# Optimization experiments

Hardware: AMD Instinct MI355X
Metric: run time of the kernel (lower is better)

The kernel has to match this reference:

```python
import jax, jax.numpy as jnp
import numpy as np

EPS = 1e-6
MAX_ITER = 3

def skew(w):
    z = jnp.zeros_like(w[:, 0])
    return jnp.stack([
        jnp.stack([z, -w[:, 2], w[:, 1]], -1),
        jnp.stack([w[:, 2], z, -w[:, 0]], -1),
        jnp.stack([-w[:, 1], w[:, 0], z], -1)], -2)

def twist2mat(w):
    # Rodrigues formula, w: [B,3] -> R: [B,3,3]
    theta = jnp.linalg.norm(w, axis=-1, keepdims=True) + 1e-12
    axis = w / theta
    Km = skew(axis)
    th = theta[..., None]
    I = jnp.eye(3, dtype=w.dtype)
    return I + jnp.sin(th) * Km + (1.0 - jnp.cos(th)) * (Km @ Km)

def sobel_gradient(img, normalize=True):
    # replicate-pad + 3x3 Sobel, img: [B,C,H,W]
    p = jnp.pad(img, ((0, 0), (0, 0), (1, 1), (1, 1)), mode='edge')
    tl = p[..., :-2, :-2]; tc = p[..., :-2, 1:-1]; tr = p[..., :-2, 2:]
    ml = p[..., 1:-1, :-2]; mr = p[..., 1:-1, 2:]
    bl = p[..., 2:, :-2]; bc = p[..., 2:, 1:-1]; br = p[..., 2:, 2:]
    dx = (tr - tl) + 2.0 * (mr - ml) + (br - bl)
    dy = (bl - tl) + 2.0 * (bc - tc) + (br - tr)
    if normalize:
        mag = jnp.sqrt(dx * dx + dy * dy + 1e-8)
        dx, dy = dx / mag, dy / mag
    return dx, dy

def _bilinear_one(F, u, v):
    # F: [C,H,W]; u,v: [H,W] pixel coords; border padding (grid_sample-like)
    C, H, W = F.shape
    u = jnp.clip(u, 0.0, W - 1.0)
    v = jnp.clip(v, 0.0, H - 1.0)
    x0 = jnp.floor(u); y0 = jnp.floor(v)
    wx = u - x0; wy = v - y0
    x0i = x0.astype(jnp.int32); y0i = y0.astype(jnp.int32)
    x1i = jnp.minimum(x0i + 1, W - 1); y1i = jnp.minimum(y0i + 1, H - 1)
    g = lambda yi, xi: F[:, yi, xi]  # advanced-index gather -> [C,H,W]
    return (g(y0i, x0i) * (1 - wx) * (1 - wy) + g(y0i, x1i) * wx * (1 - wy)
            + g(y1i, x0i) * (1 - wx) * wy + g(y1i, x1i) * wx * wy)

def warp_features(F, u, v):
    # F: [B,C,H,W]; u,v: [B,1,H,W]
    return jax.vmap(_bilinear_one)(F, u[:, 0], v[:, 0])

def generate_xy_grid(B, H, W, K):
    fx, fy, cx, cy = [K[:, i].reshape(B, 1, 1, 1) for i in range(4)]
    uu, vv = jnp.meshgrid(jnp.arange(W, dtype=K.dtype), jnp.arange(H, dtype=K.dtype))
    px = (uu[None, None] - cx) / fx
    py = (vv[None, None] - cy) / fy
    return px, py  # [B,1,H,W] each

def batch_warp_inverse_depth(px, py, invD0, R, t, K):
    B, _, H, W = px.shape
    xy1 = jnp.concatenate([px, py, jnp.ones_like(px)], 1).reshape(B, 3, -1)
    warped = R @ xy1 + t[:, :, None] * invD0.reshape(B, 1, -1)
    x_, y_, s_ = warped[:, 0], warped[:, 1], warped[:, 2]
    fx, fy, cx, cy = [K[:, i].reshape(B, 1) for i in range(4)]
    u_ = (x_ / s_ * fx + cx).reshape(B, 1, H, W)
    v_ = (y_ / s_ * fy + cy).reshape(B, 1, H, W)
    inv_z = invD0 / s_.reshape(B, 1, H, W)
    return u_, v_, inv_z

def check_occ(inv_z_buffer, invD1, u, v, thres=0.1):
    B, _, H, W = invD1.shape
    inv_z_warped = warp_features(invD1, u, v)
    inlier = inv_z_buffer > inv_z_warped - thres
    inview = (u > 0) & (u < W) & (v > 0) & (v < H)
    return ~(inlier & inview)  # [B,1,H,W] bool

def compute_jacobian_warping(invD, K, px, py):
    # linearized at origin (pose=None branch)
    B, _, H, W = invD.shape
    x = px.reshape(B, -1); y = py.reshape(B, -1); d = invD.reshape(B, -1)
    O = jnp.zeros_like(x)
    xy = x * y
    dx_dp = jnp.stack([-xy, 1.0 + x * x, -y, d, O, -d * x], -1)
    dy_dp = jnp.stack([-(1.0 + y * y), xy, x, O, d, -d * y], -1)
    fx = K[:, 0].reshape(B, 1, 1); fy = K[:, 1].reshape(B, 1, 1)
    return dx_dp * fx, dy_dp * fy  # [B,HW,6] each

def lev_mar_H(JtWJ):
    diag = jnp.eye(6, dtype=JtWJ.dtype)
    trace = jnp.trace(JtWJ, axis1=1, axis2=2)
    return JtWJ + (trace * 1e-6)[:, None, None] * diag

def forward(twist0, x0, x1, invD0, invD1, sigma0, sigma1, K):
    B, C, H, W = x0.shape
    N = H * W
    dtype = x0.dtype
    R = twist2mat(twist0[:, :3])
    t = twist0[:, 3:]
    px, py = generate_xy_grid(B, H, W, K)
    # inverse-compositional: template Jacobian precomputed once
    Jf_x, Jf_y = sobel_gradient(x0, normalize=True)
    Jx_p, Jy_p = compute_jacobian_warping(invD0, K, px, py)
    J = (Jf_x.reshape(B, C, N, 1) * Jx_p.reshape(B, 1, N, 6)
         + Jf_y.reshape(B, C, N, 1) * Jy_p.reshape(B, 1, N, 6))  # [B,C,N,6]
    for _ in range(MAX_ITER):
        u_w, v_w, inv_z = batch_warp_inverse_depth(px, py, invD0, R, t, K)
        occ = check_occ(inv_z, invD1, u_w, v_w)
        f_r = warp_features(x1, u_w, v_w)
        sigma_r = warp_features(sigma1, u_w, v_w)
        res = f_r - x0
        sigma = jnp.sqrt(sigma_r * sigma_r + sigma0 * sigma0)
        wres = jnp.where(occ, EPS, res / sigma)  # [B,C,H,W]
        valid = (~occ).reshape(B, 1, N, 1).astype(dtype)
        Jw = (J / sigma.reshape(B, C, N, 1) * valid).reshape(B, C * N, 6)
        r = jnp.where(occ, 0.0, wres).reshape(B, C * N)
        JtWJ = jnp.einsum('bnk,bnl->bkl', Jw, Jw)
        Rhs = jnp.einsum('bnk,bn->bk', Jw, r)[..., None]
        xi = jnp.linalg.solve(lev_mar_H(JtWJ), Rhs)  # [B,6,1]
        d_R = twist2mat(-xi[:, :3, 0])
        d_t = -(d_R @ xi[:, 3:])
        t = (R @ d_t)[:, :, 0] + t
        R = R @ d_R
    return jnp.concatenate([R.reshape(B, 9), t], axis=1)  # [B,12]

def setup_inputs() -> dict:
    key = jax.random.key(0)
    ks = jax.random.split(key, 7)
    B, C, H, W = 8, 16, 240, 320
    twist0 = jax.random.normal(ks[0], (B, 6), jnp.float32) * 0.01
    x0 = jax.random.normal(ks[1], (B, C, H, W), jnp.float32)
    x1 = jax.random.normal(ks[2], (B, C, H, W), jnp.float32)
    invD0 = jax.random.uniform(ks[3], (B, 1, H, W), jnp.float32, 0.1, 1.0)
    invD1 = jax.random.uniform(ks[4], (B, 1, H, W), jnp.float32, 0.1, 1.0)
    sigma0 = jax.random.uniform(ks[5], (B, C, H, W), jnp.float32, 0.1, 1.0)
    sigma1 = jax.random.uniform(ks[6], (B, C, H, W), jnp.float32, 0.1, 1.0)
    Kmat = jnp.tile(jnp.array([[0.8 * W, 0.8 * W, W / 2.0, H / 2.0]], jnp.float32), (B, 1))
    return dict(twist0=twist0, x0=x0, x1=x1, invD0=invD0, invD1=invD1,
                sigma0=sigma0, sigma1=sigma1, K=Kmat)

def reference(twist0, x0, x1, invD0, invD1, sigma0, sigma1, K):
    return forward(twist0, x0, x1, invD0, invD1, sigma0, sigma1, K)
```

## Files before the change

kernel.cpp:

```cpp
#include <hip/hip_runtime.h>
#include <hip/hip_fp16.h>

#define B_ 8
#define C_ 16
#define H_ 240
#define W_ 320
#define N_ (H_*W_)

__device__ __forceinline__ void twist2mat_dev(float w0, float w1, float w2, float R[9]) {
    float th = sqrtf(w0*w0 + w1*w1 + w2*w2) + 1e-12f;
    float ax = w0/th, ay = w1/th, az = w2/th;
    float s = sinf(th), c = cosf(th), ic = 1.0f - c;
    R[0] = 1.0f + ic*(ax*ax - 1.0f);
    R[1] = -s*az + ic*ax*ay;
    R[2] =  s*ay + ic*ax*az;
    R[3] =  s*az + ic*ax*ay;
    R[4] = 1.0f + ic*(ay*ay - 1.0f);
    R[5] = -s*ax + ic*ay*az;
    R[6] = -s*ay + ic*ax*az;
    R[7] =  s*ax + ic*ay*az;
    R[8] = 1.0f + ic*(az*az - 1.0f);
}

__device__ __forceinline__ unsigned pack_h2(float a, float b) {
    __half2 h = __floats2half2_rn(a, b);
    return *reinterpret_cast<unsigned*>(&h);
}
__device__ __forceinline__ float2 unpack_h2(unsigned u) {
    __half2 h = *reinterpret_cast<__half2*>(&u);
    return __half22float2(h);
}

__device__ __forceinline__ void solve_update(const float* __restrict__ ac, float R[9], float t[3]) {
    float M[6][7];
    {
        int idx = 0;
        #pragma unroll
        for (int k = 0; k < 6; k++)
            #pragma unroll
            for (int l = k; l < 6; l++) { M[k][l] = ac[idx]; M[l][k] = ac[idx]; idx++; }
    }
    const float trace = M[0][0]+M[1][1]+M[2][2]+M[3][3]+M[4][4]+M[5][5];
    const float lam = trace * 1e-6f;
    #pragma unroll
    for (int i = 0; i < 6; i++) { M[i][i] += lam; M[i][6] = ac[21+i]; }

    #pragma unroll
    for (int k = 0; k < 6; k++) {
        const float inv = 1.0f / M[k][k];
        #pragma unroll
        for (int i = k+1; i < 6; i++) {
            const float f = M[i][k] * inv;
            #pragma unroll
            for (int j = k; j < 7; j++) M[i][j] -= f * M[k][j];
        }
    }
    float xi[6];
    #pragma unroll
    for (int i = 5; i >= 0; i--) {
        float s = M[i][6];
        #pragma unroll
        for (int j = i+1; j < 6; j++) s -= M[i][j]*xi[j];
        xi[i] = s / M[i][i];
    }

    float dR[9];
    twist2mat_dev(-xi[0], -xi[1], -xi[2], dR);
    const float dt0 = -(dR[0]*xi[3] + dR[1]*xi[4] + dR[2]*xi[5]);
    const float dt1 = -(dR[3]*xi[3] + dR[4]*xi[4] + dR[5]*xi[5]);
    const float dt2 = -(dR[6]*xi[3] + dR[7]*xi[4] + dR[8]*xi[5]);

    const float nt0 = R[0]*dt0 + R[1]*dt1 + R[2]*dt2 + t[0];
    const float nt1 = R[3]*dt0 + R[4]*dt1 + R[5]*dt2 + t[1];
    const float nt2 = R[6]*dt0 + R[7]*dt1 + R[8]*dt2 + t[2];
    float nR[9];
    #pragma unroll
    for (int i = 0; i < 3; i++)
        #pragma unroll
        for (int j = 0; j < 3; j++)
            nR[i*3+j] = R[i*3+0]*dR[0*3+j] + R[i*3+1]*dR[1*3+j] + R[i*3+2]*dR[2*3+j];
    #pragma unroll
    for (int i = 0; i < 9; i++) R[i] = nR[i];
    t[0] = nt0; t[1] = nt1; t[2] = nt2;
}

__device__ __forceinline__ void build_RT(const float* __restrict__ twist0,
                                         const float* __restrict__ accum,
                                         int b, int iters, float R[9], float t[3]) {
    const float* w = twist0 + b*6;
    twist2mat_dev(w[0], w[1], w[2], R);
    t[0] = w[3]; t[1] = w[4]; t[2] = w[5];
    for (int j = 0; j < iters; j++)
        solve_update(accum + (size_t)(j*B_ + b)*27, R, t);
}

__launch_bounds__(256)
__global__ void precompute_kernel(const float* __restrict__ x0, const float* __restrict__ x1,
                                  const float* __restrict__ sigma0, const float* __restrict__ sigma1,
                                  uint4* __restrict__ P0h, uint4* __restrict__ X1S1h,
                                  float* __restrict__ accum)
{
    if (blockIdx.x == 0 && blockIdx.y == 0 && blockIdx.z == 0) {
        for (int k = threadIdx.x; k < 3*B_*27; k += 256) accum[k] = 0.0f;
    }
    const int b  = blockIdx.z;
    const int cg = blockIdx.y;
    const int base_pix = blockIdx.x * 256;
    const int pix = base_pix + threadIdx.x;
    const int h0 = base_pix / W_;

    __shared__ float lds[4][4][W_];

    const size_t cbase = ((size_t)(b*C_) + cg*4) * N_;

    float s0a[4], x1a[4], s1a[4];
    #pragma unroll
    for (int i = 0; i < 4; i++) {
        const size_t o = cbase + (size_t)i*N_ + pix;
        s0a[i] = sigma0[o];
        x1a[i] = x1[o];
        s1a[i] = sigma1[o];
    }

    #pragma unroll
    for (int k = 0; k < 5; k++) {
        const int idx = threadIdx.x + k*256;
        const int ch  = idx / 320;
        const int rem = idx - ch*320;
        const int row = rem / 80;
        const int c4  = rem - row*80;
        const int src_r = min(max(h0 - 1 + row, 0), H_ - 1);
        const float4 v = *reinterpret_cast<const float4*>(
            x0 + cbase + (size_t)ch*N_ + (size_t)src_r*W_ + c4*4);
        *reinterpret_cast<float4*>(&lds[ch][row][c4*4]) = v;
    }
    __syncthreads();

    const int h = pix / W_;
    const int w = pix - h*W_;
    const int lr = h - (h0 - 1);
    const int wm = max(w-1, 0), wp = min(w+1, W_-1);

    unsigned gq[4], xq[4], qq[4];
    #pragma unroll
    for (int i = 0; i < 4; i++) {
        const float* rT = lds[i][lr-1];
        const float* rM = lds[i][lr];
        const float* rB = lds[i][lr+1];
        const float tl = rT[wm], tc_ = rT[w], tr = rT[wp];
        const float ml = rM[wm], ctr = rM[w], mr = rM[wp];
        const float bl = rB[wm], bc_ = rB[w], br = rB[wp];
        const float dx = tr - tl + 2.0f*(mr - ml) + (br - bl);
        const float dy = bl - tl + 2.0f*(bc_ - tc_) + (br - tr);
        const float mag = sqrtf(dx*dx + dy*dy + 1e-8f);
        gq[i] = pack_h2(dx/mag, dy/mag);
        xq[i] = pack_h2(ctr, s0a[i]*s0a[i]);
        qq[i] = pack_h2(x1a[i], s1a[i]);
    }

    uint4 A;  A.x = gq[0];  A.y = xq[0];  A.z = gq[1];  A.w = xq[1];
    uint4 Bw; Bw.x = gq[2]; Bw.y = xq[2]; Bw.z = gq[3]; Bw.w = xq[3];
    uint4 Q;  Q.x = qq[0];  Q.y = qq[1];  Q.z = qq[2];  Q.w = qq[3];
    P0h[((size_t)(b*8 + cg*2  ))*N_ + pix] = A;
    P0h[((size_t)(b*8 + cg*2+1))*N_ + pix] = Bw;
    X1S1h[((size_t)(b*4 + cg))*N_ + pix] = Q;
}

__device__ __forceinline__ void accum_pixel(int pix,
                                            const float Rm[9], const float tv[3],
                                            float fx, float fy, float cx, float cy,
                                            const uint4* __restrict__ P0b,
                                            const uint4* __restrict__ X1S1b,
                                            const float* __restrict__ d0,
                                            const float* __restrict__ dz,
                                            float* __restrict__ acc)
{
    const int h = pix / W_;
    const int w = pix - h*W_;

    const float px = ((float)w - cx) / fx;
    const float py = ((float)h - cy) / fy;
    const float d  = d0[pix];

    const float x_ = Rm[0]*px + Rm[1]*py + Rm[2] + tv[0]*d;
    const float y_ = Rm[3]*px + Rm[4]*py + Rm[5] + tv[1]*d;
    const float s_ = Rm[6]*px + Rm[7]*py + Rm[8] + tv[2]*d;
    const float u = x_/s_*fx + cx;
    const float v = y_/s_*fy + cy;
    const float inv_z = d / s_;

    const float uc = fminf(fmaxf(u, 0.0f), (float)(W_-1));
    const float vc = fminf(fmaxf(v, 0.0f), (float)(H_-1));
    const float x0f = floorf(uc), y0f = floorf(vc);
    const float wx = uc - x0f, wy = vc - y0f;
    const int x0i = (int)x0f, y0i = (int)y0f;
    const int x1i = min(x0i+1, W_-1), y1i = min(y0i+1, H_-1);
    const float w00 = (1.0f-wx)*(1.0f-wy), w01 = wx*(1.0f-wy);
    const float w10 = (1.0f-wx)*wy,        w11 = wx*wy;
    const int i00 = y0i*W_+x0i, i01 = y0i*W_+x1i, i10 = y1i*W_+x0i, i11 = y1i*W_+x1i;

    const float zw = dz[i00]*w00 + dz[i01]*w01 + dz[i10]*w10 + dz[i11]*w11;
    const bool inlier = inv_z > zw - 0.1f;
    const bool inview = (u > 0.0f) && (u < (float)W_) && (v > 0.0f) && (v < (float)H_);
    const bool valid  = inlier && inview;

    if (!valid) return;

    const float xy = px*py;
    const float Av[6] = { -xy*fx, (1.0f+px*px)*fx, -py*fx, d*fx, 0.0f, -d*px*fx };
    const float Bv[6] = { -(1.0f+py*py)*fy, xy*fy, px*fy, 0.0f, d*fy, -d*py*fy };

    float Swxx=0.f, Swxy=0.f, Swyy=0.f, Srx=0.f, Sry=0.f;

#define CH(gword, xword, t00, t01, t10, t11) { \
    const float2 g  = unpack_h2(gword); \
    const float2 xs = unpack_h2(xword); \
    const float2 a00 = unpack_h2(t00), a01 = unpack_h2(t01), \
                 a10 = unpack_h2(t10), a11 = unpack_h2(t11); \
    const float fr = a00.x*w00 + a01.x*w01 + a10.x*w10 + a11.x*w11; \
    const float sr = a00.y*w00 + a01.y*w01 + a10.y*w10 + a11.y*w11; \
    const float inv_s2 = 1.0f/(sr*sr + xs.y); \
    const float res = fr - xs.x; \
    const float gxw = g.x*inv_s2, gyw = g.y*inv_s2; \
    Swxx += g.x*gxw; Swxy += g.x*gyw; Swyy += g.y*gyw; \
    Srx  += res*gxw; Sry  += res*gyw; }

    #pragma unroll
    for (int cg = 0; cg < 4; cg++) {
        const uint4 pA = P0b[(size_t)(cg*2  )*N_ + pix];
        const uint4 pB = P0b[(size_t)(cg*2+1)*N_ + pix];
        const uint4* xsb = X1S1b + (size_t)cg*N_;
        const uint4 q00 = xsb[i00], q01 = xsb[i01], q10 = xsb[i10], q11 = xsb[i11];
        CH(pA.x, pA.y, q00.x, q01.x, q10.x, q11.x)
        CH(pA.z, pA.w, q00.y, q01.y, q10.y, q11.y)
        CH(pB.x, pB.y, q00.z, q01.z, q10.z, q11.z)
        CH(pB.z, pB.w, q00.w, q01.w, q10.w, q11.w)
    }
#undef CH

    int idx = 0;
    #pragma unroll
    for (int k = 0; k < 6; k++) {
        #pragma unroll
        for (int l = k; l < 6; l++) {
            acc[idx++] += Swxx*Av[k]*Av[l] + Swxy*(Av[k]*Bv[l] + Bv[k]*Av[l]) + Swyy*Bv[k]*Bv[l];
        }
    }
    #pragma unroll
    for (int k = 0; k < 6; k++) acc[21+k] += Srx*Av[k] + Sry*Bv[k];
}

__launch_bounds__(256)
__global__ void iter_kernel(const uint4* __restrict__ P0h, const uint4* __restrict__ X1S1h,
                            const float* __restrict__ invD0, const float* __restrict__ invD1,
                            const float* __restrict__ Kmat, const float* __restrict__ twist0,
                            float* __restrict__ accum, int it)
{
    const int b = blockIdx.y;
    const int pix0 = blockIdx.x * 512 + threadIdx.x;

    float Rm[9], tv[3];
    build_RT(twist0, accum, b, it, Rm, tv);

    const float fx = Kmat[b*4+0], fy = Kmat[b*4+1], cx = Kmat[b*4+2], cy = Kmat[b*4+3];

    float acc[27];
    #pragma unroll
    for (int j = 0; j < 27; j++) acc[j] = 0.0f;

    const uint4* P0b   = P0h   + (size_t)b*8*N_;
    const uint4* X1S1b = X1S1h + (size_t)b*4*N_;
    const float* d0 = invD0 + b*N_;
    const float* dz = invD1 + b*N_;

    accum_pixel(pix0,       Rm, tv, fx, fy, cx, cy, P0b, X1S1b, d0, dz, acc);
    accum_pixel(pix0 + 256, Rm, tv, fx, fy, cx, cy, P0b, X1S1b, d0, dz, acc);

    const int lane = threadIdx.x & 63;
    const int wave = threadIdx.x >> 6;
    __shared__ float red[4][27];
    #pragma unroll
    for (int j = 0; j < 27; j++) {
        float vv = acc[j];
        vv += __shfl_down(vv, 32);
        vv += __shfl_down(vv, 16);
        vv += __shfl_down(vv, 8);
        vv += __shfl_down(vv, 4);
        vv += __shfl_down(vv, 2);
        vv += __shfl_down(vv, 1);
        if (lane == 0) red[wave][j] = vv;
    }
    __syncthreads();
    if (threadIdx.x < 27) {
        float s = red[0][threadIdx.x] + red[1][threadIdx.x] + red[2][threadIdx.x] + red[3][threadIdx.x];
        atomicAdd(&accum[(size_t)(it*B_ + b)*27 + threadIdx.x], s);
    }
}

__global__ void finalize_kernel(const float* __restrict__ twist0, const float* __restrict__ accum,
                                float* __restrict__ out)
{
    const int b = threadIdx.x;
    if (b >= B_) return;
    float Rm[9], tv[3];
    build_RT(twist0, accum, b, 3, Rm, tv);
    float* ob = out + b*12;
    #pragma unroll
    for (int i = 0; i < 9; i++) ob[i] = Rm[i];
    ob[9] = tv[0]; ob[10] = tv[1]; ob[11] = tv[2];
}

extern "C" void kernel_launch(void* const* d_in, const int* in_sizes, int n_in,
                              void* d_out, int out_size, void* d_ws, size_t ws_size,
                              hipStream_t stream) {
    const float* twist0 = (const float*)d_in[0];
    const float* x0     = (const float*)d_in[1];
    const float* x1     = (const float*)d_in[2];
    const float* invD0  = (const float*)d_in[3];
    const float* invD1  = (const float*)d_in[4];
    const float* sigma0 = (const float*)d_in[5];
    const float* sigma1 = (const float*)d_in[6];
    const float* Kmat   = (const float*)d_in[7];
    float* out = (float*)d_out;

    const size_t p0_bytes = (size_t)B_*8*N_*sizeof(uint4);
    const size_t xs_bytes = (size_t)B_*4*N_*sizeof(uint4);

    uint4* P0h   = (uint4*)d_ws;
    uint4* X1S1h = (uint4*)((char*)d_ws + p0_bytes);
    float* accum = (float*)((char*)d_ws + p0_bytes + xs_bytes);

    hipLaunchKernelGGL(precompute_kernel, dim3(N_/256, 4, B_), dim3(256), 0, stream,
                       x0, x1, sigma0, sigma1, P0h, X1S1h, accum);

    dim3 grid(N_/512, B_);
    for (int it = 0; it < 3; ++it) {
        hipLaunchKernelGGL(iter_kernel, grid, dim3(256), 0, stream,
                           P0h, X1S1h, invD0, invD1, Kmat, twist0, accum, it);
    }
    hipLaunchKernelGGL(finalize_kernel, dim3(1), dim3(64), 0, stream, twist0, accum, out);
}
```

Baseline: 335.6 us.

## Split iteration kernel across channel groups with four pixels per thread

The iteration kernel now gives each block one channel group (4 of 16 channels) instead of all channels, and each thread handles four pixels instead of two. Grid rows become batch times channel groups, while the pixel blocks per row are halved. Each thread holds fewer live gather loads per pixel, which may help occupancy and latency hiding. The cost is that the geometry, projection and Jacobian work is repeated four times per pixel, and the 6x6 accumulation plus atomic reduction now runs per channel group.

```diff
diff --git a/kernel.cpp b/kernel.cpp
--- a/kernel.cpp
+++ b/kernel.cpp
@@ -166,14 +166,14 @@
     X1S1h[((size_t)(b*4 + cg))*N_ + pix] = Q;
 }
 
-__device__ __forceinline__ void accum_pixel(int pix,
-                                            const float Rm[9], const float tv[3],
-                                            float fx, float fy, float cx, float cy,
-                                            const uint4* __restrict__ P0b,
-                                            const uint4* __restrict__ X1S1b,
-                                            const float* __restrict__ d0,
-                                            const float* __restrict__ dz,
-                                            float* __restrict__ acc)
+__device__ __forceinline__ void accum_pixel_cg(int pix,
+                                               const float Rm[9], const float tv[3],
+                                               float fx, float fy, float cx, float cy,
+                                               const uint4* __restrict__ P0cg,
+                                               const uint4* __restrict__ X1cg,
+                                               const float* __restrict__ d0,
+                                               const float* __restrict__ dz,
+                                               float* __restrict__ acc)
 {
     const int h = pix / W_;
     const int w = pix - h*W_;
@@ -225,12 +225,10 @@
     Swxx += g.x*gxw; Swxy += g.x*gyw; Swyy += g.y*gyw; \
     Srx  += res*gxw; Sry  += res*gyw; }
 
-    #pragma unroll
-    for (int cg = 0; cg < 4; cg++) {
-        const uint4 pA = P0b[(size_t)(cg*2  )*N_ + pix];
-        const uint4 pB = P0b[(size_t)(cg*2+1)*N_ + pix];
-        const uint4* xsb = X1S1b + (size_t)cg*N_;
-        const uint4 q00 = xsb[i00], q01 = xsb[i01], q10 = xsb[i10], q11 = xsb[i11];
+    {
+        const uint4 pA = P0cg[pix];
+        const uint4 pB = P0cg[N_ + pix];
+        const uint4 q00 = X1cg[i00], q01 = X1cg[i01], q10 = X1cg[i10], q11 = X1cg[i11];
         CH(pA.x, pA.y, q00.x, q01.x, q10.x, q11.x)
         CH(pA.z, pA.w, q00.y, q01.y, q10.y, q11.y)
         CH(pB.x, pB.y, q00.z, q01.z, q10.z, q11.z)
@@ -256,8 +254,9 @@
                             const float* __restrict__ Kmat, const float* __restrict__ twist0,
                             float* __restrict__ accum, int it)
 {
-    const int b = blockIdx.y;
-    const int pix0 = blockIdx.x * 512 + threadIdx.x;
+    const int b  = blockIdx.y >> 2;
+    const int cg = blockIdx.y & 3;
+    const int pix0 = blockIdx.x * 1024 + threadIdx.x;
 
     float Rm[9], tv[3];
     build_RT(twist0, accum, b, it, Rm, tv);
@@ -268,13 +267,15 @@
     #pragma unroll
     for (int j = 0; j < 27; j++) acc[j] = 0.0f;
 
-    const uint4* P0b   = P0h   + (size_t)b*8*N_;
-    const uint4* X1S1b = X1S1h + (size_t)b*4*N_;
+    const uint4* P0cg = P0h   + (size_t)(b*8 + cg*2)*N_;
+    const uint4* X1cg = X1S1h + (size_t)(b*4 + cg  )*N_;
     const float* d0 = invD0 + b*N_;
     const float* dz = invD1 + b*N_;
 
-    accum_pixel(pix0,       Rm, tv, fx, fy, cx, cy, P0b, X1S1b, d0, dz, acc);
-    accum_pixel(pix0 + 256, Rm, tv, fx, fy, cx, cy, P0b, X1S1b, d0, dz, acc);
+    accum_pixel_cg(pix0,       Rm, tv, fx, fy, cx, cy, P0cg, X1cg, d0, dz, acc);
+    accum_pixel_cg(pix0 + 256, Rm, tv, fx, fy, cx, cy, P0cg, X1cg, d0, dz, acc);
+    accum_pixel_cg(pix0 + 512, Rm, tv, fx, fy, cx, cy, P0cg, X1cg, d0, dz, acc);
+    accum_pixel_cg(pix0 + 768, Rm, tv, fx, fy, cx, cy, P0cg, X1cg, d0, dz, acc);
 
     const int lane = threadIdx.x & 63;
     const int wave = threadIdx.x >> 6;
@@ -333,7 +334,7 @@
     hipLaunchKernelGGL(precompute_kernel, dim3(N_/256, 4, B_), dim3(256), 0, stream,
                        x0, x1, sigma0, sigma1, P0h, X1S1h, accum);
 
-    dim3 grid(N_/512, B_);
+    dim3 grid(N_/1024, B_*4);
     for (int it = 0; it < 3; ++it) {
         hipLaunchKernelGGL(iter_kernel, grid, dim3(256), 0, stream,
                            P0h, X1S1h, invD0, invD1, Kmat, twist0, accum, it);
```

Result: slower. 381.7 us (+13.7%).

## Interleave two pixels per thread and replace validity branch with mask

Applied to the files above, without the earlier changes.

The per-pixel function that handled two pixels one after another, with an early return for invalid pixels, is split into warp setup and per-channel accumulation. Both pixels' gathers are now issued together, which raises memory-level parallelism. The validity branch becomes a multiplicative mask, so invalid pixels still do all loads and math but divergence is removed. This raises register pressure and adds redundant gathers for invalid pixels.

```diff
diff --git a/kernel.cpp b/kernel.cpp
--- a/kernel.cpp
+++ b/kernel.cpp
@@ -166,88 +166,54 @@
     X1S1h[((size_t)(b*4 + cg))*N_ + pix] = Q;
 }
 
-__device__ __forceinline__ void accum_pixel(int pix,
-                                            const float Rm[9], const float tv[3],
-                                            float fx, float fy, float cx, float cy,
-                                            const uint4* __restrict__ P0b,
-                                            const uint4* __restrict__ X1S1b,
-                                            const float* __restrict__ d0,
-                                            const float* __restrict__ dz,
-                                            float* __restrict__ acc)
-{
+struct Warp {
+    int i00, i01, i10, i11;
+    float w00, w01, w10, w11;
+    float inv_z;
+    float px, py;
+    bool  inview;
+};
+
+__device__ __forceinline__ Warp make_warp(int pix, float d, const float Rm[9], const float tv[3],
+                                          float fx, float fy, float cx, float cy) {
+    Warp W;
     const int h = pix / W_;
     const int w = pix - h*W_;
-
-    const float px = ((float)w - cx) / fx;
-    const float py = ((float)h - cy) / fy;
-    const float d  = d0[pix];
-
-    const float x_ = Rm[0]*px + Rm[1]*py + Rm[2] + tv[0]*d;
-    const float y_ = Rm[3]*px + Rm[4]*py + Rm[5] + tv[1]*d;
-    const float s_ = Rm[6]*px + Rm[7]*py + Rm[8] + tv[2]*d;
+    W.px = ((float)w - cx) / fx;
+    W.py = ((float)h - cy) / fy;
+    const float x_ = Rm[0]*W.px + Rm[1]*W.py + Rm[2] + tv[0]*d;
+    const float y_ = Rm[3]*W.px + Rm[4]*W.py + Rm[5] + tv[1]*d;
+    const float s_ = Rm[6]*W.px + Rm[7]*W.py + Rm[8] + tv[2]*d;
     const float u = x_/s_*fx + cx;
     const float v = y_/s_*fy + cy;
-    const float inv_z = d / s_;
-
+    W.inv_z = d / s_;
     const float uc = fminf(fmaxf(u, 0.0f), (float)(W_-1));
     const float vc = fminf(fmaxf(v, 0.0f), (float)(H_-1));
     const float x0f = floorf(uc), y0f = floorf(vc);
     const float wx = uc - x0f, wy = vc - y0f;
     const int x0i = (int)x0f, y0i = (int)y0f;
     const int x1i = min(x0i+1, W_-1), y1i = min(y0i+1, H_-1);
-    const float w00 = (1.0f-wx)*(1.0f-wy), w01 = wx*(1.0f-wy);
-    const float w10 = (1.0f-wx)*wy,        w11 = wx*wy;
-    const int i00 = y0i*W_+x0i, i01 = y0i*W_+x1i, i10 = y1i*W_+x0i, i11 = y1i*W_+x1i;
-
-    const float zw = dz[i00]*w00 + dz[i01]*w01 + dz[i10]*w10 + dz[i11]*w11;
-    const bool inlier = inv_z > zw - 0.1f;
-    const bool inview = (u > 0.0f) && (u < (float)W_) && (v > 0.0f) && (v < (float)H_);
-    const bool valid  = inlier && inview;
-
-    if (!valid) return;
-
-    const float xy = px*py;
-    const float Av[6] = { -xy*fx, (1.0f+px*px)*fx, -py*fx, d*fx, 0.0f, -d*px*fx };
-    const float Bv[6] = { -(1.0f+py*py)*fy, xy*fy, px*fy, 0.0f, d*fy, -d*py*fy };
-
-    float Swxx=0.f, Swxy=0.f, Swyy=0.f, Srx=0.f, Sry=0.f;
-
-#define CH(gword, xword, t00, t01, t10, t11) { \
-    const float2 g  = unpack_h2(gword); \
-    const float2 xs = unpack_h2(xword); \
-    const float2 a00 = unpack_h2(t00), a01 = unpack_h2(t01), \
-                 a10 = unpack_h2(t10), a11 = unpack_h2(t11); \
-    const float fr = a00.x*w00 + a01.x*w01 + a10.x*w10 + a11.x*w11; \
-    const float sr = a00.y*w00 + a01.y*w01 + a10.y*w10 + a11.y*w11; \
-    const float inv_s2 = 1.0f/(sr*sr + xs.y); \
-    const float res = fr - xs.x; \
-    const float gxw = g.x*inv_s2, gyw = g.y*inv_s2; \
-    Swxx += g.x*gxw; Swxy += g.x*gyw; Swyy += g.y*gyw; \
-    Srx  += res*gxw; Sry  += res*gyw; }
-
-    #pragma unroll
-    for (int cg = 0; cg < 4; cg++) {
-        const uint4 pA = P0b[(size_t)(cg*2  )*N_ + pix];
-        const uint4 pB = P0b[(size_t)(cg*2+1)*N_ + pix];
-        const uint4* xsb = X1S1b + (size_t)cg*N_;
-        const uint4 q00 = xsb[i00], q01 = xsb[i01], q10 = xsb[i10], q11 = xsb[i11];
-        CH(pA.x, pA.y, q00.x, q01.x, q10.x, q11.x)
-        CH(pA.z, pA.w, q00.y, q01.y, q10.y, q11.y)
-        CH(pB.x, pB.y, q00.z, q01.z, q10.z, q11.z)
-        CH(pB.z, pB.w, q00.w, q01.w, q10.w, q11.w)
-    }
-#undef CH
-
-    int idx = 0;
-    #pragma unroll
-    for (int k = 0; k < 6; k++) {
-        #pragma unroll
-        for (int l = k; l < 6; l++) {
-            acc[idx++] += Swxx*Av[k]*Av[l] + Swxy*(Av[k]*Bv[l] + Bv[k]*Av[l]) + Swyy*Bv[k]*Bv[l];
-        }
-    }
-    #pragma unroll
-    for (int k = 0; k < 6; k++) acc[21+k] += Srx*Av[k] + Sry*Bv[k];
+    W.w00 = (1.0f-wx)*(1.0f-wy); W.w01 = wx*(1.0f-wy);
+    W.w10 = (1.0f-wx)*wy;        W.w11 = wx*wy;
+    W.i00 = y0i*W_+x0i; W.i01 = y0i*W_+x1i; W.i10 = y1i*W_+x0i; W.i11 = y1i*W_+x1i;
+    W.inview = (u > 0.0f) && (u < (float)W_) && (v > 0.0f) && (v < (float)H_);
+    return W;
+}
+
+__device__ __forceinline__ void ch_accum(const Warp& W, float S[5],
+                                         unsigned gword, unsigned xword,
+                                         unsigned t00, unsigned t01, unsigned t10, unsigned t11) {
+    const float2 g  = unpack_h2(gword);
+    const float2 xs = unpack_h2(xword);
+    const float2 a00 = unpack_h2(t00), a01 = unpack_h2(t01),
+                 a10 = unpack_h2(t10), a11 = unpack_h2(t11);
+    const float fr = a00.x*W.w00 + a01.x*W.w01 + a10.x*W.w10 + a11.x*W.w11;
+    const float sr = a00.y*W.w00 + a01.y*W.w01 + a10.y*W.w10 + a11.y*W.w11;
+    const float inv_s2 = 1.0f/(sr*sr + xs.y);
+    const float res = fr - xs.x;
+    const float gxw = g.x*inv_s2, gyw = g.y*inv_s2;
+    S[0] += g.x*gxw; S[1] += g.x*gyw; S[2] += g.y*gyw;
+    S[3] += res*gxw; S[4] += res*gyw;
 }
 
 __launch_bounds__(256)
@@ -257,24 +223,89 @@
                             float* __restrict__ accum, int it)
 {
     const int b = blockIdx.y;
-    const int pix0 = blockIdx.x * 512 + threadIdx.x;
+    const int pixA = blockIdx.x * 512 + threadIdx.x;
+    const int pixB = pixA + 256;
 
     float Rm[9], tv[3];
     build_RT(twist0, accum, b, it, Rm, tv);
 
     const float fx = Kmat[b*4+0], fy = Kmat[b*4+1], cx = Kmat[b*4+2], cy = Kmat[b*4+3];
 
-    float acc[27];
-    #pragma unroll
-    for (int j = 0; j < 27; j++) acc[j] = 0.0f;
-
+    const float* d0 = invD0 + b*N_;
+    const float* dz = invD1 + b*N_;
     const uint4* P0b   = P0h   + (size_t)b*8*N_;
     const uint4* X1S1b = X1S1h + (size_t)b*4*N_;
-    const float* d0 = invD0 + b*N_;
-    const float* dz = invD1 + b*N_;
-
-    accum_pixel(pix0,       Rm, tv, fx, fy, cx, cy, P0b, X1S1b, d0, dz, acc);
-    accum_pixel(pix0 + 256, Rm, tv, fx, fy, cx, cy, P0b, X1S1b, d0, dz, acc);
+
+    const float dA = d0[pixA];
+    const float dB = d0[pixB];
+
+    const Warp A = make_warp(pixA, dA, Rm, tv, fx, fy, cx, cy);
+    const Warp B = make_warp(pixB, dB, Rm, tv, fx, fy, cx, cy);
+
+    const float zA00 = dz[A.i00], zA01 = dz[A.i01], zA10 = dz[A.i10], zA11 = dz[A.i11];
+    const float zB00 = dz[B.i00], zB01 = dz[B.i01], zB10 = dz[B.i10], zB11 = dz[B.i11];
+    const float zwA = zA00*A.w00 + zA01*A.w01 + zA10*A.w10 + zA11*A.w11;
+    const float zwB = zB00*B.w00 + zB01*B.w01 + zB10*B.w10 + zB11*B.w11;
+    const float vmA = (A.inv_z > zwA - 0.1f && A.inview) ? 1.0f : 0.0f;
+    const float vmB = (B.inv_z > zwB - 0.1f && B.inview) ? 1.0f : 0.0f;
+
+    float SA[5] = {0.f,0.f,0.f,0.f,0.f};
+    float SB[5] = {0.f,0.f,0.f,0.f,0.f};
+
+    #pragma unroll
+    for (int cg = 0; cg < 4; cg++) {
+        const uint4 pAa = P0b[(size_t)(cg*2  )*N_ + pixA];
+        const uint4 pAb = P0b[(size_t)(cg*2+1)*N_ + pixA];
+        const uint4 pBa = P0b[(size_t)(cg*2  )*N_ + pixB];
+        const uint4 pBb = P0b[(size_t)(cg*2+1)*N_ + pixB];
+        const uint4* xsb = X1S1b + (size_t)cg*N_;
+        const uint4 qA00 = xsb[A.i00], qA01 = xsb[A.i01], qA10 = xsb[A.i10], qA11 = xsb[A.i11];
+        const uint4 qB00 = xsb[B.i00], qB01 = xsb[B.i01], qB10 = xsb[B.i10], qB11 = xsb[B.i11];
+
+        ch_accum(A, SA, pAa.x, pAa.y, qA00.x, qA01.x, qA10.x, qA11.x);
+        ch_accum(A, SA, pAa.z, pAa.w, qA00.y, qA01.y, qA10.y, qA11.y);
+        ch_accum(A, SA, pAb.x, pAb.y, qA00.z, qA01.z, qA10.z, qA11.z);
+        ch_accum(A, SA, pAb.z, pAb.w, qA00.w, qA01.w, qA10.w, qA11.w);
+
+        ch_accum(B, SB, pBa.x, pBa.y, qB00.x, qB01.x, qB10.x, qB11.x);
+        ch_accum(B, SB, pBa.z, pBa.w, qB00.y, qB01.y, qB10.y, qB11.y);
+        ch_accum(B, SB, pBb.x, pBb.y, qB00.z, qB01.z, qB10.z, qB11.z);
+        ch_accum(B, SB, pBb.z, pBb.w, qB00.w, qB01.w, qB10.w, qB11.w);
+    }
+
+    #pragma unroll
+    for (int k = 0; k < 5; k++) { SA[k] *= vmA; SB[k] *= vmB; }
+
+    float AvA[6], BvA[6], AvB[6], BvB[6];
+    {
+        const float xyA = A.px*A.py;
+        AvA[0] = -xyA*fx; AvA[1] = (1.0f+A.px*A.px)*fx; AvA[2] = -A.py*fx;
+        AvA[3] = dA*fx;   AvA[4] = 0.0f;                AvA[5] = -dA*A.px*fx;
+        BvA[0] = -(1.0f+A.py*A.py)*fy; BvA[1] = xyA*fy; BvA[2] = A.px*fy;
+        BvA[3] = 0.0f;    BvA[4] = dA*fy;               BvA[5] = -dA*A.py*fy;
+        const float xyB = B.px*B.py;
+        AvB[0] = -xyB*fx; AvB[1] = (1.0f+B.px*B.px)*fx; AvB[2] = -B.py*fx;
+        AvB[3] = dB*fx;   AvB[4] = 0.0f;                AvB[5] = -dB*B.px*fx;
+        BvB[0] = -(1.0f+B.py*B.py)*fy; BvB[1] = xyB*fy; BvB[2] = B.px*fy;
+        BvB[3] = 0.0f;    BvB[4] = dB*fy;               BvB[5] = -dB*B.py*fy;
+    }
+
+    float acc[27];
+    {
+        int idx = 0;
+        #pragma unroll
+        for (int k = 0; k < 6; k++) {
+            #pragma unroll
+            for (int l = k; l < 6; l++) {
+                acc[idx++] =
+                    SA[0]*AvA[k]*AvA[l] + SA[1]*(AvA[k]*BvA[l] + BvA[k]*AvA[l]) + SA[2]*BvA[k]*BvA[l] +
+                    SB[0]*AvB[k]*AvB[l] + SB[1]*(AvB[k]*BvB[l] + BvB[k]*AvB[l]) + SB[2]*BvB[k]*BvB[l];
+            }
+        }
+        #pragma unroll
+        for (int k = 0; k < 6; k++)
+            acc[21+k] = SA[3]*AvA[k] + SA[4]*BvA[k] + SB[3]*AvB[k] + SB[4]*BvB[k];
+    }
 
     const int lane = threadIdx.x & 63;
     const int wave = threadIdx.x >> 6;
```

Result: slower. 419.8 us (+25.1%).
